# Kernel tuning notes

Hardware: AMD Instinct MI355X
Metric: run time of the kernel (lower is better)

## Reference

```python
import jax, jax.numpy as jnp
import numpy as np

B, T, D, H, MLP, NI, OUT = 256, 2049, 64, 64, 128, 128, 10
L = D + D * (D - 1) // 2  # depth-2 logsignature channels = 2080


def _logsig_depth2(X, n_intervals):
    """Depth-2 log-signature of a piecewise-linear path over equal intervals.
    X: [B, T, D] with T = n_intervals*s + 1. Returns [B, n_intervals, L] where
    L = D + D(D-1)/2 (level-1 increments + strictly-upper-triangular Levy areas,
    the Lyndon-word basis signatory uses at depth 2)."""
    Bq, Tq, Dq = X.shape
    s = (Tq - 1) // n_intervals
    idx = np.arange(n_intervals)[:, None] * s + np.arange(s + 1)[None, :]
    seg = X[:, idx]                       # [B, n, s+1, D]
    inc = seg[:, :, -1] - seg[:, :, 0]    # level 1: [B, n, D]
    dlt = seg[:, :, 1:] - seg[:, :, :-1]  # per-step increments [B, n, s, D]
    cum = seg[:, :, :-1] - seg[:, :, :1]  # partial increments  [B, n, s, D]
    M = jnp.einsum('bnki,bnkj->bnij', cum, dlt)
    A = 0.5 * (M - jnp.swapaxes(M, -1, -2))  # Levy area [B, n, D, D]
    iu, ju = np.triu_indices(Dq, 1)
    return jnp.concatenate([inc, A[..., iu, ju]], axis=-1)  # [B, n, L]


def setup_inputs() -> dict:
    key = jax.random.key(0)
    ks = jax.random.split(key, 10)
    X = jax.random.normal(ks[0], (B, T, D), jnp.float32) * 0.05
    W_in = jax.random.normal(ks[1], (D, H), jnp.float32) / np.sqrt(D)
    b_in = jnp.zeros((H,), jnp.float32)
    W1 = jax.random.normal(ks[2], (H, MLP), jnp.float32) / np.sqrt(H)
    b1 = jnp.zeros((MLP,), jnp.float32)
    W2 = jax.random.normal(ks[3], (MLP, D * L), jnp.float32) / np.sqrt(MLP)
    b2 = jnp.zeros((D * L,), jnp.float32)
    W_out = jax.random.normal(ks[4], (H, OUT), jnp.float32) / np.sqrt(H)
    b_out = jnp.zeros((OUT,), jnp.float32)
    return {"X": X, "W_in": W_in, "b_in": b_in, "W1": W1, "b1": b1,
            "W2": W2, "b2": b2, "W_out": W_out, "b_out": b_out,
            "n_intervals": NI}


def reference(X, W_in, b_in, W1, b1, W2, b2, W_out, b_out, n_intervals):
    Bq, Tq, Dq = X.shape
    logsig = _logsig_depth2(X, n_intervals)        # [B, n, L]
    h0 = X[:, 0] @ W_in + b_in                     # initial_linear

    def vf(h):  # F.forward: MLP(h) -> [B, D, L]
        z = jnp.tanh(h @ W1 + b1)
        return (z @ W2 + b2).reshape(Bq, Dq, -1)

    def g(h, ls):  # f(h) contracted with logsig derivative
        return jnp.einsum('bdl,bl->bd', vf(h), ls)

    def rk4_step(h, ls):  # one RK4 step per interval, dt = 1
        k1 = g(h, ls)
        k2 = g(h + 0.5 * k1, ls)
        k3 = g(h + 0.5 * k2, ls)
        k4 = g(h + k3, ls)
        return h + (k1 + 2.0 * k2 + 2.0 * k3 + k4) / 6.0, None

    hT, _ = jax.lax.scan(rk4_step, h0, jnp.swapaxes(logsig, 0, 1))
    return hT @ W_out + b_out  # readout_linear: [B, OUT]
```

## Files before the change

kernel.cpp:

```cpp
#include <hip/hip_runtime.h>
#include <hip/hip_bf16.h>
#include <cstdint>
#include <cstddef>

#define B_SZ   256
#define T_SZ   2049
#define D_SZ   64
#define H_SZ   64
#define MLP_SZ 128
#define NI_SZ  128
#define SEG    16
#define L_SZ   2080
#define NPAIR  2016
#define OUT_SZ 10

#define NC     32
#define NCHUNK (NI_SZ / NC)
#define MROWS  (NC * B_SZ)
#define NCOLS  8320
#define KDIM   L_SZ

typedef _Float16 f16x8 __attribute__((ext_vector_type(8)));
typedef float    f32x4 __attribute__((ext_vector_type(4)));

__device__ __forceinline__ float rlane(float v, int l) {
    return __uint_as_float(__builtin_amdgcn_readlane(__float_as_uint(v), l));
}

__global__ __launch_bounds__(256) void build_B(const float* __restrict__ W2,
                                               const float* __restrict__ b2,
                                               _Float16* __restrict__ Bm) {
    const int r = blockIdx.x, t = threadIdx.x;
    const float* src = nullptr;
    if (r < 8192) {
        const int d = r >> 7, m = r & 127;
        src = W2 + (size_t)m * (64 * KDIM) + (size_t)d * KDIM;
    } else if (r < 8256) {
        src = b2 + (size_t)(r - 8192) * KDIM;
    }
    _Float16* dst = Bm + (size_t)r * KDIM;
    for (int l = t; l < KDIM; l += 256)
        dst[l] = src ? (_Float16)src[l] : (_Float16)0.0f;
}

__global__ void h0_kernel(const float* __restrict__ X, const float* __restrict__ W_in,
                          const float* __restrict__ b_in, float* __restrict__ h_state) {
    const int b = blockIdx.x, t = threadIdx.x;
    __shared__ float x0[D_SZ];
    if (t < D_SZ) x0[t] = X[(size_t)b * T_SZ * D_SZ + t];
    __syncthreads();
    float acc = b_in[t];
    for (int k = 0; k < D_SZ; ++k) acc += x0[k] * W_in[k * H_SZ + t];
    h_state[b * H_SZ + t] = acc;
}

__global__ __launch_bounds__(256) void logsig_kernel(const float* __restrict__ X,
                                                     _Float16* __restrict__ LS,
                                                     int n0) {
    const int b = blockIdx.x, sl = blockIdx.y, t = threadIdx.x;
    const int n = n0 + sl;
    __shared__ float seg[SEG + 1][D_SZ];
    __shared__ float cum[SEG][D_SZ];
    __shared__ float dlt[SEG][D_SZ];
    __shared__ float Mm[D_SZ][D_SZ + 1];

    const float* Xp = X + ((size_t)b * T_SZ + (size_t)n * SEG) * D_SZ;
    for (int i = t; i < (SEG + 1) * D_SZ / 4; i += 256)
        ((float4*)&seg[0][0])[i] = ((const float4*)Xp)[i];
    __syncthreads();
    for (int i = t; i < SEG * D_SZ; i += 256) {
        const int k = i >> 6, d = i & 63;
        cum[k][d] = seg[k][d] - seg[0][d];
        dlt[k][d] = seg[k + 1][d] - seg[k][d];
    }
    __syncthreads();

    const int ti = t >> 4, tj = t & 15;
    const int i0 = ti * 4, j0 = tj * 4;
    float m4[4][4] = {};
#pragma unroll
    for (int k = 0; k < SEG; ++k) {
        const float4 ci = *(const float4*)&cum[k][i0];
        const float4 dj = *(const float4*)&dlt[k][j0];
        const float* cip = (const float*)&ci;
        const float* djp = (const float*)&dj;
#pragma unroll
        for (int a = 0; a < 4; ++a)
#pragma unroll
            for (int c = 0; c < 4; ++c)
                m4[a][c] += cip[a] * djp[c];
    }
#pragma unroll
    for (int a = 0; a < 4; ++a)
#pragma unroll
        for (int c = 0; c < 4; ++c)
            Mm[i0 + a][j0 + c] = m4[a][c];
    __syncthreads();

    _Float16* out = LS + (size_t)(sl * B_SZ + b) * KDIM;
    if (t < D_SZ) out[t] = (_Float16)(seg[SEG][t] - seg[0][t]);
    if (tj >= ti) {
#pragma unroll
        for (int a = 0; a < 4; ++a) {
            const int i = i0 + a;
#pragma unroll
            for (int c = 0; c < 4; ++c) {
                const int j = j0 + c;
                if (j > i) {
                    const int p = 63 * i - (i * (i - 1)) / 2 + (j - i - 1);
                    out[D_SZ + p] = (_Float16)(0.5f * (m4[a][c] - Mm[j][i]));
                }
            }
        }
    }
}

__global__ __launch_bounds__(256) void gemm_bt(const unsigned short* __restrict__ A,
                                               const unsigned short* __restrict__ Bm,
                                               _Float16* __restrict__ C) {
    constexpr int K = KDIM, N = NCOLS;
    __shared__ unsigned short As[128 * 32];
    __shared__ unsigned short Bs[128 * 32];
    const int t = threadIdx.x;
    const int lane = t & 63;
    const int w = t >> 6;
    const int wm = w & 1, wn = w >> 1;
    const int tileM = blockIdx.x * 128;
    const int tileN = blockIdx.y * 128;

    const int c0 = w * 2, c1 = c0 + 1;
    const int rs0 = c0 * 16 + (lane >> 2);
    const int rs1 = c1 * 16 + (lane >> 2);
    const int kc = (((lane & 3) ^ ((lane >> 2) & 3))) * 8;

    const unsigned short* gA0 = A + (size_t)(tileM + rs0) * K + kc;
    const unsigned short* gA1 = A + (size_t)(tileM + rs1) * K + kc;
    const unsigned short* gB0 = Bm + (size_t)(tileN + rs0) * K + kc;
    const unsigned short* gB1 = Bm + (size_t)(tileN + rs1) * K + kc;
    unsigned short* lA0 = As + c0 * 512 + lane * 8;
    unsigned short* lA1 = As + c1 * 512 + lane * 8;
    unsigned short* lB0 = Bs + c0 * 512 + lane * 8;
    unsigned short* lB1 = Bs + c1 * 512 + lane * 8;

    f32x4 acc[4][4] = {};
    const int frow = lane & 15;
    const int fkswz = (((lane >> 4) ^ (frow & 3))) * 8;

    for (int k0 = 0; k0 < K; k0 += 32) {
        __syncthreads();
        __builtin_amdgcn_global_load_lds((__attribute__((address_space(1))) void*)(gA0 + k0),
                                         (__attribute__((address_space(3))) void*)lA0, 16, 0, 0);
        __builtin_amdgcn_global_load_lds((__attribute__((address_space(1))) void*)(gA1 + k0),
                                         (__attribute__((address_space(3))) void*)lA1, 16, 0, 0);
        __builtin_amdgcn_global_load_lds((__attribute__((address_space(1))) void*)(gB0 + k0),
                                         (__attribute__((address_space(3))) void*)lB0, 16, 0, 0);
        __builtin_amdgcn_global_load_lds((__attribute__((address_space(1))) void*)(gB1 + k0),
                                         (__attribute__((address_space(3))) void*)lB1, 16, 0, 0);
        __syncthreads();

        f16x8 af[4], bfm[4];
#pragma unroll
        for (int mi = 0; mi < 4; ++mi)
            af[mi] = *(const f16x8*)(As + (wm * 64 + mi * 16 + frow) * 32 + fkswz);
#pragma unroll
        for (int ni = 0; ni < 4; ++ni)
            bfm[ni] = *(const f16x8*)(Bs + (wn * 64 + ni * 16 + frow) * 32 + fkswz);
#pragma unroll
        for (int mi = 0; mi < 4; ++mi)
#pragma unroll
            for (int ni = 0; ni < 4; ++ni)
                acc[mi][ni] = __builtin_amdgcn_mfma_f32_16x16x32_f16(af[mi], bfm[ni],
                                                                     acc[mi][ni], 0, 0, 0);
    }

    const int erow = (lane >> 4) * 4;
#pragma unroll
    for (int mi = 0; mi < 4; ++mi)
#pragma unroll
        for (int ni = 0; ni < 4; ++ni) {
            const int col = tileN + wn * 64 + ni * 16 + frow;
            const size_t rbase = (size_t)(tileM + wm * 64 + mi * 16 + erow) * N + col;
#pragma unroll
            for (int r = 0; r < 4; ++r)
                C[rbase + (size_t)r * N] = (_Float16)acc[mi][ni][r];
        }
}

__global__ __launch_bounds__(256) void ode_chunk(const _Float16* __restrict__ G,
                                                 const float* __restrict__ W1,
                                                 const float* __restrict__ b1,
                                                 float* __restrict__ h_state) {
    const int b = blockIdx.x, t = threadIdx.x;
    const int lane = t & 63, w = t >> 6;
    const int j0 = w * 32 + (lane & 31);
    __shared__ float ysw[4][D_SZ];
    __shared__ float part[2][4][D_SZ];

    float w1c[D_SZ];
#pragma unroll
    for (int dd = 0; dd < D_SZ; ++dd) w1c[dd] = W1[dd * MLP_SZ + j0];
    const float b1v = b1[j0];

    float hsv = h_state[b * H_SZ + lane];
    ysw[w][lane] = hsv;
    float k_st[4] = {0.f, 0.f, 0.f, 0.f};

    f16x8 pr[4];
    _Float16 b2pre;
    {
        const _Float16* Gr = G + (size_t)b * NCOLS;
        const f16x8* gp = (const f16x8*)(Gr + lane * 128 + w * 32);
#pragma unroll
        for (int v = 0; v < 4; ++v) pr[v] = gp[v];
        b2pre = Gr[8192 + lane];
    }

#pragma unroll 1
    for (int s = 0; s < NC; ++s) {
        float gcur[32];
#pragma unroll
        for (int v = 0; v < 4; ++v)
#pragma unroll
            for (int e = 0; e < 8; ++e) gcur[v * 8 + e] = (float)pr[v][e];
        const float b2cur = (float)b2pre;
        if (s + 1 < NC) {
            const _Float16* Gr = G + (size_t)((s + 1) * B_SZ + b) * NCOLS;
            const f16x8* gp = (const f16x8*)(Gr + lane * 128 + w * 32);
#pragma unroll
            for (int v = 0; v < 4; ++v) pr[v] = gp[v];
            b2pre = Gr[8192 + lane];
        }

#pragma unroll
        for (int st = 0; st < 4; ++st) {
            float a = 0.0f;
#pragma unroll
            for (int dd = 0; dd < D_SZ; dd += 4) {
                const float4 yv = *(const float4*)&ysw[w][dd];
                a += yv.x * w1c[dd] + yv.y * w1c[dd + 1]
                   + yv.z * w1c[dd + 2] + yv.w * w1c[dd + 3];
            }
            const float x = b1v + a;
            const float ex = __expf(2.0f * x);
            const float z = 1.0f - 2.0f / (ex + 1.0f);
            float a2 = 0.0f;
#pragma unroll
            for (int q = 0; q < 32; ++q)
                a2 += gcur[q] * rlane(z, q);
            part[st & 1][w][lane] = a2;
            __syncthreads();
            const float kv = b2cur + part[st & 1][0][lane] + part[st & 1][1][lane]
                           + part[st & 1][2][lane] + part[st & 1][3][lane];
            k_st[st] = kv;
            if (st < 3) {
                float y = hsv;
                if (st == 0) y += 0.5f * kv;
                else if (st == 1) y += 0.5f * kv;
                else y += kv;
                ysw[w][lane] = y;
            }
        }
        hsv += (k_st[0] + 2.0f * k_st[1] + 2.0f * k_st[2] + k_st[3]) * (1.0f / 6.0f);
        ysw[w][lane] = hsv;
    }
    if (w == 0) h_state[b * H_SZ + lane] = hsv;
}

__global__ void out_kernel(const float* __restrict__ h_state, const float* __restrict__ W_out,
                           const float* __restrict__ b_out, float* __restrict__ out) {
    const int b = blockIdx.x, t = threadIdx.x;
    __shared__ float hh[H_SZ];
    hh[t] = h_state[b * H_SZ + t];
    __syncthreads();
    if (t < OUT_SZ) {
        float acc = b_out[t];
        for (int d = 0; d < H_SZ; ++d) acc += hh[d] * W_out[d * OUT_SZ + t];
        out[b * OUT_SZ + t] = acc;
    }
}

extern "C" void kernel_launch(void* const* d_in, const int* in_sizes, int n_in,
                              void* d_out, int out_size, void* d_ws, size_t ws_size,
                              hipStream_t stream) {
    (void)in_sizes; (void)n_in; (void)out_size; (void)ws_size;
    const float* X     = (const float*)d_in[0];
    const float* W_in  = (const float*)d_in[1];
    const float* b_in  = (const float*)d_in[2];
    const float* W1    = (const float*)d_in[3];
    const float* b1    = (const float*)d_in[4];
    const float* W2    = (const float*)d_in[5];
    const float* b2    = (const float*)d_in[6];
    const float* W_out = (const float*)d_in[7];
    const float* b_out = (const float*)d_in[8];
    float* out = (float*)d_out;

    char* ws = (char*)d_ws;
    size_t off = 0;
    auto take = [&](size_t bytes) { void* p = ws + off; off = (off + bytes + 255) & ~(size_t)255; return p; };
    _Float16* Bmat = (_Float16*)take((size_t)NCOLS * KDIM * 2);
    _Float16* LSc  = (_Float16*)take((size_t)MROWS * KDIM * 2);
    _Float16* G    = (_Float16*)take((size_t)MROWS * NCOLS * 2);
    float*    hst  = (float*)take((size_t)B_SZ * H_SZ * 4);

    build_B<<<NCOLS, 256, 0, stream>>>(W2, b2, Bmat);
    h0_kernel<<<B_SZ, H_SZ, 0, stream>>>(X, W_in, b_in, hst);

    for (int c = 0; c < NCHUNK; ++c) {
        logsig_kernel<<<dim3(B_SZ, NC), 256, 0, stream>>>(X, LSc, c * NC);
        gemm_bt<<<dim3(MROWS / 128, NCOLS / 128), 256, 0, stream>>>(
            (const unsigned short*)LSc, (const unsigned short*)Bmat, G);
        ode_chunk<<<B_SZ, 256, 0, stream>>>(G, W1, b1, hst);
    }
    out_kernel<<<B_SZ, H_SZ, 0, stream>>>(hst, W_out, b_out, out);
}
```

Before: 2.246 ms.

## Replace 128x128 GEMM with double-buffered 256x256 MFMA kernel and padded K

Rewrites the main fp16 GEMM as a 512-thread, 256x256-tile kernel that double-buffers 64-wide K slices in LDS through direct global-to-LDS loads, with explicit waitcnt/barrier scheduling and setprio around the MFMA bursts. K is padded to 2112 and N to 8448 so every tile is full, the output is written with an 8256-column stride that skips the padding, and workgroups are remapped so neighbouring blocks share tiles in L2. The goal is more data reuse per LDS byte and load latency hidden behind MFMA work, at the cost of higher register and LDS pressure and some wasted compute on the padding.

```diff
diff --git a/kernel.cpp b/kernel.cpp
--- a/kernel.cpp
+++ b/kernel.cpp
@@ -10,15 +10,16 @@
 #define MLP_SZ 128
 #define NI_SZ  128
 #define SEG    16
-#define L_SZ   2080
-#define NPAIR  2016
+#define KDIM   2080
+#define KP     2112
 #define OUT_SZ 10
 
 #define NC     32
 #define NCHUNK (NI_SZ / NC)
 #define MROWS  (NC * B_SZ)
-#define NCOLS  8320
-#define KDIM   L_SZ
+#define NB     8448
+#define GSTR   8256
+#define NT     (KP / 64)
 
 typedef _Float16 f16x8 __attribute__((ext_vector_type(8)));
 typedef float    f32x4 __attribute__((ext_vector_type(4)));
@@ -38,9 +39,9 @@
     } else if (r < 8256) {
         src = b2 + (size_t)(r - 8192) * KDIM;
     }
-    _Float16* dst = Bm + (size_t)r * KDIM;
-    for (int l = t; l < KDIM; l += 256)
-        dst[l] = src ? (_Float16)src[l] : (_Float16)0.0f;
+    _Float16* dst = Bm + (size_t)r * KP;
+    for (int l = t; l < KP; l += 256)
+        dst[l] = (src && l < KDIM) ? (_Float16)src[l] : (_Float16)0.0f;
 }
 
 __global__ void h0_kernel(const float* __restrict__ X, const float* __restrict__ W_in,
@@ -97,8 +98,9 @@
             Mm[i0 + a][j0 + c] = m4[a][c];
     __syncthreads();
 
-    _Float16* out = LS + (size_t)(sl * B_SZ + b) * KDIM;
+    _Float16* out = LS + (size_t)(sl * B_SZ + b) * KP;
     if (t < D_SZ) out[t] = (_Float16)(seg[SEG][t] - seg[0][t]);
+    if (t < KP - KDIM) out[KDIM + t] = (_Float16)0.0f;
     if (tj >= ti) {
 #pragma unroll
         for (int a = 0; a < 4; ++a) {
@@ -115,75 +117,140 @@
     }
 }
 
-__global__ __launch_bounds__(256) void gemm_bt(const unsigned short* __restrict__ A,
-                                               const unsigned short* __restrict__ Bm,
-                                               _Float16* __restrict__ C) {
-    constexpr int K = KDIM, N = NCOLS;
-    __shared__ unsigned short As[128 * 32];
-    __shared__ unsigned short Bs[128 * 32];
+#define GLDS(SRC, DST) __builtin_amdgcn_global_load_lds(                        \
+    (__attribute__((address_space(1))) void*)(SRC),                             \
+    (__attribute__((address_space(3))) void*)(DST), 16, 0, 0)
+
+#define STAGE(KT, KK, BUF) do {                                                 \
+    const unsigned short* _sa = Asrc + (size_t)(KT) * 64 + (KK) * 32;           \
+    const unsigned short* _sb = Bsrc + (size_t)(KT) * 64 + (KK) * 32;           \
+    unsigned short* _d = ldst + (BUF) * 32768 + (KK) * 8192;                    \
+    GLDS(_sa,                  _d);                                             \
+    GLDS(_sa + (size_t)128*KP, _d + 4096);                                      \
+    GLDS(_sb,                  _d + 16384);                                     \
+    GLDS(_sb + (size_t)128*KP, _d + 20480);                                     \
+} while (0)
+
+#define BAR() do { __builtin_amdgcn_s_barrier(); __builtin_amdgcn_sched_barrier(0); } while (0)
+
+#define VMW_(N) asm volatile("s_waitcnt vmcnt(" #N ")" ::: "memory")
+#define VMW(N) VMW_(N)
+
+#define LOAD_A(KK, MB) do {                                                     \
+    af0 = *(const f16x8*)(aC + (KK) * 8192 + ((MB) + 0) * 512);                 \
+    af1 = *(const f16x8*)(aC + (KK) * 8192 + ((MB) + 1) * 512);                 \
+    af2 = *(const f16x8*)(aC + (KK) * 8192 + ((MB) + 2) * 512);                 \
+    af3 = *(const f16x8*)(aC + (KK) * 8192 + ((MB) + 3) * 512);                 \
+} while (0)
+
+#define LOAD_B(KK) do {                                                         \
+    bg0 = *(const f16x8*)(bC + (KK) * 8192 + 0 * 512);                          \
+    bg1 = *(const f16x8*)(bC + (KK) * 8192 + 1 * 512);                          \
+    bg2 = *(const f16x8*)(bC + (KK) * 8192 + 2 * 512);                          \
+    bg3 = *(const f16x8*)(bC + (KK) * 8192 + 3 * 512);                          \
+} while (0)
+
+#define MFMA16(MB) do {                                                         \
+    __builtin_amdgcn_s_setprio(1);                                              \
+    acc[(MB)+0][0] = __builtin_amdgcn_mfma_f32_16x16x32_f16(af0, bg0, acc[(MB)+0][0], 0, 0, 0); \
+    acc[(MB)+0][1] = __builtin_amdgcn_mfma_f32_16x16x32_f16(af0, bg1, acc[(MB)+0][1], 0, 0, 0); \
+    acc[(MB)+1][0] = __builtin_amdgcn_mfma_f32_16x16x32_f16(af1, bg0, acc[(MB)+1][0], 0, 0, 0); \
+    acc[(MB)+1][1] = __builtin_amdgcn_mfma_f32_16x16x32_f16(af1, bg1, acc[(MB)+1][1], 0, 0, 0); \
+    acc[(MB)+0][2] = __builtin_amdgcn_mfma_f32_16x16x32_f16(af0, bg2, acc[(MB)+0][2], 0, 0, 0); \
+    acc[(MB)+0][3] = __builtin_amdgcn_mfma_f32_16x16x32_f16(af0, bg3, acc[(MB)+0][3], 0, 0, 0); \
+    acc[(MB)+1][2] = __builtin_amdgcn_mfma_f32_16x16x32_f16(af1, bg2, acc[(MB)+1][2], 0, 0, 0); \
+    acc[(MB)+1][3] = __builtin_amdgcn_mfma_f32_16x16x32_f16(af1, bg3, acc[(MB)+1][3], 0, 0, 0); \
+    acc[(MB)+2][0] = __builtin_amdgcn_mfma_f32_16x16x32_f16(af2, bg0, acc[(MB)+2][0], 0, 0, 0); \
+    acc[(MB)+2][1] = __builtin_amdgcn_mfma_f32_16x16x32_f16(af2, bg1, acc[(MB)+2][1], 0, 0, 0); \
+    acc[(MB)+3][0] = __builtin_amdgcn_mfma_f32_16x16x32_f16(af3, bg0, acc[(MB)+3][0], 0, 0, 0); \
+    acc[(MB)+3][1] = __builtin_amdgcn_mfma_f32_16x16x32_f16(af3, bg1, acc[(MB)+3][1], 0, 0, 0); \
+    acc[(MB)+2][2] = __builtin_amdgcn_mfma_f32_16x16x32_f16(af2, bg2, acc[(MB)+2][2], 0, 0, 0); \
+    acc[(MB)+2][3] = __builtin_amdgcn_mfma_f32_16x16x32_f16(af2, bg3, acc[(MB)+2][3], 0, 0, 0); \
+    acc[(MB)+3][2] = __builtin_amdgcn_mfma_f32_16x16x32_f16(af3, bg2, acc[(MB)+3][2], 0, 0, 0); \
+    acc[(MB)+3][3] = __builtin_amdgcn_mfma_f32_16x16x32_f16(af3, bg3, acc[(MB)+3][3], 0, 0, 0); \
+    __builtin_amdgcn_s_setprio(0);                                              \
+} while (0)
+
+#define TILE_BODY(TT, CUR, DOS1, DOS0, V1, V2) do {                             \
+    const unsigned short* aC = aP + (CUR) * 32768;                              \
+    const unsigned short* bC = bP + (CUR) * 32768;                              \
+                                  \
+    if (DOS1) { STAGE((TT) + 1, 1, (CUR) ^ 1); }                                \
+    LOAD_B(0); LOAD_A(0, 0);                                                    \
+    BAR(); MFMA16(0); BAR();                                                    \
+                                                                        \
+    LOAD_A(0, 4);                                                               \
+    BAR(); MFMA16(4); VMW(V1); BAR();                                           \
+                                    \
+    if (DOS0) { STAGE((TT) + 2, 0, (CUR)); }                                    \
+    LOAD_B(1); LOAD_A(1, 0);                                                    \
+    BAR(); MFMA16(0); BAR();                                                    \
+                                                                        \
+    LOAD_A(1, 4);                                                               \
+    BAR(); MFMA16(4); VMW(V2); BAR();                                           \
+} while (0)
+
+__global__ __launch_bounds__(512, 2) void gemm256(const unsigned short* __restrict__ A,
+                                                  const unsigned short* __restrict__ Bm,
+                                                  _Float16* __restrict__ C) {
+    __shared__ unsigned short lds[65536];
     const int t = threadIdx.x;
-    const int lane = t & 63;
-    const int w = t >> 6;
-    const int wm = w & 1, wn = w >> 1;
-    const int tileM = blockIdx.x * 128;
-    const int tileN = blockIdx.y * 128;
-
-    const int c0 = w * 2, c1 = c0 + 1;
-    const int rs0 = c0 * 16 + (lane >> 2);
-    const int rs1 = c1 * 16 + (lane >> 2);
-    const int kc = (((lane & 3) ^ ((lane >> 2) & 3))) * 8;
-
-    const unsigned short* gA0 = A + (size_t)(tileM + rs0) * K + kc;
-    const unsigned short* gA1 = A + (size_t)(tileM + rs1) * K + kc;
-    const unsigned short* gB0 = Bm + (size_t)(tileN + rs0) * K + kc;
-    const unsigned short* gB1 = Bm + (size_t)(tileN + rs1) * K + kc;
-    unsigned short* lA0 = As + c0 * 512 + lane * 8;
-    unsigned short* lA1 = As + c1 * 512 + lane * 8;
-    unsigned short* lB0 = Bs + c0 * 512 + lane * 8;
-    unsigned short* lB1 = Bs + c1 * 512 + lane * 8;
-
-    f32x4 acc[4][4] = {};
-    const int frow = lane & 15;
-    const int fkswz = (((lane >> 4) ^ (frow & 3))) * 8;
-
-    for (int k0 = 0; k0 < K; k0 += 32) {
-        __syncthreads();
-        __builtin_amdgcn_global_load_lds((__attribute__((address_space(1))) void*)(gA0 + k0),
-                                         (__attribute__((address_space(3))) void*)lA0, 16, 0, 0);
-        __builtin_amdgcn_global_load_lds((__attribute__((address_space(1))) void*)(gA1 + k0),
-                                         (__attribute__((address_space(3))) void*)lA1, 16, 0, 0);
-        __builtin_amdgcn_global_load_lds((__attribute__((address_space(1))) void*)(gB0 + k0),
-                                         (__attribute__((address_space(3))) void*)lB0, 16, 0, 0);
-        __builtin_amdgcn_global_load_lds((__attribute__((address_space(1))) void*)(gB1 + k0),
-                                         (__attribute__((address_space(3))) void*)lB1, 16, 0, 0);
-        __syncthreads();
-
-        f16x8 af[4], bfm[4];
-#pragma unroll
-        for (int mi = 0; mi < 4; ++mi)
-            af[mi] = *(const f16x8*)(As + (wm * 64 + mi * 16 + frow) * 32 + fkswz);
-#pragma unroll
-        for (int ni = 0; ni < 4; ++ni)
-            bfm[ni] = *(const f16x8*)(Bs + (wn * 64 + ni * 16 + frow) * 32 + fkswz);
-#pragma unroll
-        for (int mi = 0; mi < 4; ++mi)
-#pragma unroll
-            for (int ni = 0; ni < 4; ++ni)
-                acc[mi][ni] = __builtin_amdgcn_mfma_f32_16x16x32_f16(af[mi], bfm[ni],
-                                                                     acc[mi][ni], 0, 0, 0);
-    }
-
-    const int erow = (lane >> 4) * 4;
-#pragma unroll
-    for (int mi = 0; mi < 4; ++mi)
+
+    const int wg = blockIdx.x;
+    const int x  = (wg & 7) * 132 + (wg >> 3);
+    const int bx = x / 33, by = x % 33;
+    const int tileM = bx * 256, tileN = by * 256;
+
+    const int q7 = (t >> 3) & 7;
+    const int u  = (t & 7) ^ q7;
+    const int strow = ((t >> 3) << 1) + (u >> 2);
+    const int stcol = (u & 3) << 3;
+    const unsigned short* Asrc = A  + (size_t)(tileM + strow) * KP + stcol;
+    const unsigned short* Bsrc = Bm + (size_t)(tileN + strow) * KP + stcol;
+    unsigned short* ldst = lds + t * 8;
+
+    const int lane = t & 63, w = t >> 6;
+    const int wm = w >> 2, wn = w & 3;
+    const int frow = lane & 15, j4 = lane >> 4;
+    const int fr2 = frow >> 1;
+    const int slot = (((frow & 1) << 2) | j4) ^ fr2;
+    const unsigned short* aP = lds + wm * 4096 + fr2 * 64 + slot * 8;
+    const unsigned short* bP = lds + 16384 + wn * 2048 + fr2 * 64 + slot * 8;
+
+    f32x4 acc[8][4] = {};
+    f16x8 af0, af1, af2, af3, bg0, bg1, bg2, bg3;
+
+    STAGE(0, 0, 0);
+    STAGE(0, 1, 0);
+    STAGE(1, 0, 1);
+    VMW(8);
+    BAR();
+
+    int cur = 0;
+#pragma unroll 1
+    for (int tt = 0; tt < NT - 2; ++tt) {
+        TILE_BODY(tt, cur, 1, 1, 8, 8);
+        cur ^= 1;
+    }
+    TILE_BODY(NT - 2, cur, 1, 0, 8, 4);
+    cur ^= 1;
+    TILE_BODY(NT - 1, cur, 0, 0, 0, 0);
+
+    const int erow = j4 << 2;
+#pragma unroll
+    for (int mi = 0; mi < 8; ++mi) {
+        const int grow = tileM + wm * 128 + mi * 16 + erow;
 #pragma unroll
         for (int ni = 0; ni < 4; ++ni) {
-            const int col = tileN + wn * 64 + ni * 16 + frow;
-            const size_t rbase = (size_t)(tileM + wm * 64 + mi * 16 + erow) * N + col;
-#pragma unroll
-            for (int r = 0; r < 4; ++r)
-                C[rbase + (size_t)r * N] = (_Float16)acc[mi][ni][r];
+            const int gcol = tileN + wn * 64 + ni * 16 + frow;
+            if (gcol < GSTR) {
+                _Float16* cp = C + (size_t)grow * GSTR + gcol;
+#pragma unroll
+                for (int r = 0; r < 4; ++r)
+                    cp[(size_t)r * GSTR] = (_Float16)acc[mi][ni][r];
+            }
         }
+    }
 }
 
 __global__ __launch_bounds__(256) void ode_chunk(const _Float16* __restrict__ G,
@@ -208,7 +275,7 @@
     f16x8 pr[4];
     _Float16 b2pre;
     {
-        const _Float16* Gr = G + (size_t)b * NCOLS;
+        const _Float16* Gr = G + (size_t)b * GSTR;
         const f16x8* gp = (const f16x8*)(Gr + lane * 128 + w * 32);
 #pragma unroll
         for (int v = 0; v < 4; ++v) pr[v] = gp[v];
@@ -224,7 +291,7 @@
             for (int e = 0; e < 8; ++e) gcur[v * 8 + e] = (float)pr[v][e];
         const float b2cur = (float)b2pre;
         if (s + 1 < NC) {
-            const _Float16* Gr = G + (size_t)((s + 1) * B_SZ + b) * NCOLS;
+            const _Float16* Gr = G + (size_t)((s + 1) * B_SZ + b) * GSTR;
             const f16x8* gp = (const f16x8*)(Gr + lane * 128 + w * 32);
 #pragma unroll
             for (int v = 0; v < 4; ++v) pr[v] = gp[v];
@@ -297,17 +364,17 @@
     char* ws = (char*)d_ws;
     size_t off = 0;
     auto take = [&](size_t bytes) { void* p = ws + off; off = (off + bytes + 255) & ~(size_t)255; return p; };
-    _Float16* Bmat = (_Float16*)take((size_t)NCOLS * KDIM * 2);
-    _Float16* LSc  = (_Float16*)take((size_t)MROWS * KDIM * 2);
-    _Float16* G    = (_Float16*)take((size_t)MROWS * NCOLS * 2);
+    _Float16* Bmat = (_Float16*)take((size_t)NB * KP * 2);
+    _Float16* LSc  = (_Float16*)take((size_t)MROWS * KP * 2);
+    _Float16* G    = (_Float16*)take((size_t)MROWS * GSTR * 2);
     float*    hst  = (float*)take((size_t)B_SZ * H_SZ * 4);
 
-    build_B<<<NCOLS, 256, 0, stream>>>(W2, b2, Bmat);
+    build_B<<<NB, 256, 0, stream>>>(W2, b2, Bmat);
     h0_kernel<<<B_SZ, H_SZ, 0, stream>>>(X, W_in, b_in, hst);
 
     for (int c = 0; c < NCHUNK; ++c) {
         logsig_kernel<<<dim3(B_SZ, NC), 256, 0, stream>>>(X, LSc, c * NC);
-        gemm_bt<<<dim3(MROWS / 128, NCOLS / 128), 256, 0, stream>>>(
+        gemm256<<<dim3(32 * 33), 512, 0, stream>>>(
             (const unsigned short*)LSc, (const unsigned short*)Bmat, G);
         ode_chunk<<<B_SZ, 256, 0, stream>>>(G, W1, b1, hst);
     }
```

Measured after the change: 1.987 ms. 11.5% less time.
